# Kernel tuning notes

Measured on AMD Instinct MI355X. Metric: run time of the kernel, lower is better.

## Reference

```python
import jax, jax.numpy as jnp
import numpy as np

H = 8
DK = 16  # 128 // 8
DM = 128


def setup_inputs() -> dict:
    key = jax.random.key(0)
    ks = jax.random.split(key, 12)
    B, S = 4, 2048
    inp = {
        "query": jax.random.normal(ks[0], (B, S, DM), dtype=jnp.float32),
        "key": jax.random.normal(ks[1], (B, S, DM), dtype=jnp.float32),
        "value": jax.random.normal(ks[2], (B, S, DM), dtype=jnp.float32),
        "pos_embed": jax.random.normal(ks[3], (B, S, DM), dtype=jnp.float32),
        # three projection linears (shared: L0 for pos_query & query, L1 for pos_key & key, L2 for value)
        "W0": jax.random.normal(ks[4], (DM, DM), dtype=jnp.float32) / np.sqrt(DM),
        "b0": jnp.zeros((DM,), dtype=jnp.float32),
        "W1": jax.random.normal(ks[5], (DM, DM), dtype=jnp.float32) / np.sqrt(DM),
        "b1": jnp.zeros((DM,), dtype=jnp.float32),
        "W2": jax.random.normal(ks[6], (DM, DM), dtype=jnp.float32) / np.sqrt(DM),
        "b2": jnp.zeros((DM,), dtype=jnp.float32),
        "Wo": jax.random.normal(ks[7], (DM, DM), dtype=jnp.float32) / np.sqrt(DM),
        "bo": jnp.zeros((DM,), dtype=jnp.float32),
    }
    return inp


def _proj(x, W, b):
    # Linear then split heads: [B,S,128] -> [B,H,S,DK]
    B = x.shape[0]
    y = x @ W.T + b
    return y.reshape(B, -1, H, DK).transpose(0, 2, 1, 3)


def reference(query, key, value, pos_embed, W0, b0, W1, b1, W2, b2, Wo, bo):
    B = query.shape[0]
    pos1 = pos_embed[..., 0:DM]
    pos_q = _proj(pos1, W0, b0)  # shares L0 with query proj (as in source zip bug)
    pos_k = _proj(pos1, W1, b1)
    pos_attn = jnp.einsum("bhqd,bhkd->bhqk", pos_q, pos_k)  # [B,H,S,S]

    q = _proj(query, W0, b0)
    k = _proj(key, W1, b1)
    v = _proj(value, W2, b2)

    scale = 1.0 / jnp.sqrt(jnp.asarray(DK, dtype=q.dtype))
    scores = jnp.einsum("bhqd,bhkd->bhqk", q, k) * scale + pos_attn
    attn = jax.nn.softmax(scores, axis=-1)  # dropout = identity (eval)
    x = jnp.einsum("bhqk,bhkd->bhqd", attn, v)  # [B,H,S,DK]
    x = x.transpose(0, 2, 1, 3).reshape(B, -1, H * DK)
    return x @ Wo.T + bo
```

## Files before the change

kernel.cpp:

```cpp
#include <hip/hip_runtime.h>
#include <math.h>

#define LOG2E 1.44269504088896340736f

typedef __attribute__((ext_vector_type(8))) short bfrag;
typedef __attribute__((ext_vector_type(4))) float f4;
typedef unsigned __attribute__((ext_vector_type(2))) u2;

__device__ __forceinline__ unsigned pk_trunc(float a, float b) {
#if __has_builtin(__builtin_amdgcn_perm)
    return __builtin_amdgcn_perm(__float_as_uint(b), __float_as_uint(a), 0x07060302u);
#else
    return (__float_as_uint(a) >> 16) | (__float_as_uint(b) & 0xFFFF0000u);
#endif
}
__device__ __forceinline__ unsigned pk_rne(float a, float b) {
    unsigned ua = __float_as_uint(a); ua += 0x7FFFu + ((ua >> 16) & 1u);
    unsigned ub = __float_as_uint(b); ub += 0x7FFFu + ((ub >> 16) & 1u);
    return (ua >> 16) | (ub & 0xFFFF0000u);
}
__device__ __forceinline__ float trunchi(float x) {
    return __uint_as_float(__float_as_uint(x) & 0xFFFF0000u);
}
__device__ __forceinline__ float fexp2(float x) {
#if __has_builtin(__builtin_amdgcn_exp2f)
    return __builtin_amdgcn_exp2f(x);
#else
    return exp2f(x);
#endif
}
__device__ __forceinline__ void stage16(void* lds_base, const void* g) {
#if __has_builtin(__builtin_amdgcn_global_load_lds)
    __builtin_amdgcn_global_load_lds(
        (const __attribute__((address_space(1))) unsigned int*)g,
        (__attribute__((address_space(3))) unsigned int*)lds_base, 16, 0, 0);
#else
    int lane = threadIdx.x & 63;
    *(float4*)((char*)lds_base + lane * 16) = *(const float4*)g;
#endif
}
__device__ __forceinline__ f4 mfma_bf16(bfrag a, bfrag b, f4 c) {
    return __builtin_amdgcn_mfma_f32_16x16x32_bf16(a, b, c, 0, 0, 0);
}
__device__ __forceinline__ void conv8(const float* __restrict__ g, bfrag& hi, bfrag& lo) {
    f4 a = *(const f4*)g;
    f4 b = *(const f4*)(g + 4);
    union { unsigned u[4]; bfrag v; } H, L;
    H.u[0] = pk_trunc(a.x, a.y); H.u[1] = pk_trunc(a.z, a.w);
    H.u[2] = pk_trunc(b.x, b.y); H.u[3] = pk_trunc(b.z, b.w);
    L.u[0] = pk_trunc(a.x - trunchi(a.x), a.y - trunchi(a.y));
    L.u[1] = pk_trunc(a.z - trunchi(a.z), a.w - trunchi(a.w));
    L.u[2] = pk_trunc(b.x - trunchi(b.x), b.y - trunchi(b.y));
    L.u[3] = pk_trunc(b.z - trunchi(b.z), b.w - trunchi(b.w));
    hi = H.v; lo = L.v;
}
__device__ __forceinline__ void store_q2(f4 ea, f4 eb, char* base, int lodelta, int lane) {
    union { unsigned u[4]; bfrag v; } H, L;
    H.u[0] = pk_trunc(ea[0], ea[1]); H.u[1] = pk_trunc(ea[2], ea[3]);
    H.u[2] = pk_trunc(eb[0], eb[1]); H.u[3] = pk_trunc(eb[2], eb[3]);
    L.u[0] = pk_trunc(ea[0] - trunchi(ea[0]), ea[1] - trunchi(ea[1]));
    L.u[1] = pk_trunc(ea[2] - trunchi(ea[2]), ea[3] - trunchi(ea[3]));
    L.u[2] = pk_trunc(eb[0] - trunchi(eb[0]), eb[1] - trunchi(eb[1]));
    L.u[3] = pk_trunc(eb[2] - trunchi(eb[2]), eb[3] - trunchi(eb[3]));
    *(bfrag*)(base + lane * 16) = H.v;
    *(bfrag*)(base + lodelta + lane * 16) = L.v;
}
__device__ __forceinline__ void store_rne2(f4 ea, f4 eb, char* base, int lane) {
    union { unsigned u[4]; bfrag v; } P;
    P.u[0] = pk_rne(ea[0], ea[1]); P.u[1] = pk_rne(ea[2], ea[3]);
    P.u[2] = pk_rne(eb[0], eb[1]); P.u[3] = pk_rne(eb[2], eb[3]);
    *(bfrag*)(base + lane * 16) = P.v;
}

#define WS_QB 0u
#define WS_KV 8388608u
#define WS_X  14680064u
#define WS_WI 18874368u

__global__ __launch_bounds__(256) void w_prep(
    const float* __restrict__ W0, const float* __restrict__ W1,
    const float* __restrict__ W2, const float* __restrict__ Wo,
    char* __restrict__ wimg)
{
    int wid = blockIdx.x * 4 + (threadIdx.x >> 6);
    int lane = threadIdx.x & 63;
    int img = wid >> 5, rem = wid & 31, tile = rem >> 2, kg = rem & 3;
    const float* W = (img <= 1) ? W0 : (img == 2) ? W1 : (img == 3) ? W2 : Wo;
    float s = (img == 0) ? 0.25f * LOG2E : (img == 1) ? LOG2E : 1.0f;
    int n = lane & 15, qd = lane >> 4;
    const float* rowp = W + (size_t)(tile * 16 + n) * 128 + kg * 32;
    f4 a, b;
    if (img == 4) { a = *(const f4*)(rowp + qd * 4); b = *(const f4*)(rowp + 16 + qd * 4); }
    else          { a = *(const f4*)(rowp + qd * 8); b = *(const f4*)(rowp + qd * 8 + 4); }
    a.x *= s; a.y *= s; a.z *= s; a.w *= s;
    b.x *= s; b.y *= s; b.z *= s; b.w *= s;
    union { unsigned u[4]; bfrag v; } H, L;
    H.u[0] = pk_trunc(a.x, a.y); H.u[1] = pk_trunc(a.z, a.w);
    H.u[2] = pk_trunc(b.x, b.y); H.u[3] = pk_trunc(b.z, b.w);
    L.u[0] = pk_trunc(a.x - trunchi(a.x), a.y - trunchi(a.y));
    L.u[1] = pk_trunc(a.z - trunchi(a.z), a.w - trunchi(a.w));
    L.u[2] = pk_trunc(b.x - trunchi(b.x), b.y - trunchi(b.y));
    L.u[3] = pk_trunc(b.z - trunchi(b.z), b.w - trunchi(b.w));
    char* dst = wimg + img * 65536 + tile * 8192 + kg * 2048;
    *(bfrag*)(dst + lane * 16) = H.v;
    *(bfrag*)(dst + 1024 + lane * 16) = L.v;
}

__global__ __launch_bounds__(256) void k_proj(
    const float* __restrict__ query, const float* __restrict__ key,
    const float* __restrict__ value, const float* __restrict__ pos,
    const float* __restrict__ b0, const float* __restrict__ b1,
    const float* __restrict__ b2,
    const char* __restrict__ wimg, char* __restrict__ qb, char* __restrict__ kv)
{
    __shared__ __align__(16) char xlds[65536];
    const int tid = threadIdx.x;
    const int bid = blockIdx.x;
    const int b = bid >> 6, s32 = bid & 63;
    const size_t rowbase = (size_t)(b * 2048 + s32 * 32);

#pragma unroll
    for (int i = 0; i < 8; ++i) {
        int cid = tid + i * 256;
        int arr = cid >> 9, rem = cid & 511;
        int c32 = rem >> 4, u = rem & 15;
        const float* sp = (arr == 0) ? query : (arr == 1) ? key
                        : (arr == 2) ? value : pos;
        bfrag hi, lo;
        conv8(sp + (rowbase + c32) * 128 + u * 8, hi, lo);
        int base = arr * 16384 + (c32 >> 4) * 8192 + (u >> 2) * 2048
                 + ((u & 3) * 16 + (c32 & 15)) * 16;
        *(bfrag*)(xlds + base) = hi;
        *(bfrag*)(xlds + base + 1024) = lo;
    }
    __syncthreads();

    const int w = tid >> 6, lane = tid & 63;
    const int n = lane & 15, qd = lane >> 4;
#pragma unroll
    for (int hh = 0; hh < 2; ++hh) {
        const int h = w * 2 + hh;
        const int bh = b * 8 + h;
        {
            bfrag wqh[4], wql[4], wph[4], wpl[4];
#pragma unroll
            for (int kg = 0; kg < 4; ++kg) {
                const char* wb = wimg + 0 * 65536 + h * 8192 + kg * 2048;
                wqh[kg] = *(const bfrag*)(wb + lane * 16);
                wql[kg] = *(const bfrag*)(wb + 1024 + lane * 16);
                const char* pb = wimg + 1 * 65536 + h * 8192 + kg * 2048;
                wph[kg] = *(const bfrag*)(pb + lane * 16);
                wpl[kg] = *(const bfrag*)(pb + 1024 + lane * 16);
            }
            float bq[4], bp[4];
#pragma unroll
            for (int r = 0; r < 4; ++r) {
                float bv = b0[h * 16 + qd * 4 + r];
                bq[r] = 0.25f * LOG2E * bv; bp[r] = LOG2E * bv;
            }
#pragma unroll
            for (int pp = 0; pp < 2; ++pp) {
                f4 cq = {bq[0], bq[1], bq[2], bq[3]};
                f4 cp = {bp[0], bp[1], bp[2], bp[3]};
#pragma unroll
                for (int kg = 0; kg < 4; ++kg) {
                    const char* xq = xlds + 0 * 16384 + pp * 8192 + kg * 2048 + lane * 16;
                    const char* xp = xlds + 3 * 16384 + pp * 8192 + kg * 2048 + lane * 16;
                    bfrag xh = *(const bfrag*)xq, xl = *(const bfrag*)(xq + 1024);
                    bfrag ph = *(const bfrag*)xp, pl = *(const bfrag*)(xp + 1024);
                    cq = mfma_bf16(wqh[kg], xh, cq);
                    cq = mfma_bf16(wqh[kg], xl, cq);
                    cq = mfma_bf16(wql[kg], xh, cq);
                    cp = mfma_bf16(wph[kg], ph, cp);
                    cp = mfma_bf16(wph[kg], pl, cp);
                    cp = mfma_bf16(wpl[kg], ph, cp);
                }
                int pg = s32 * 2 + pp;
                store_q2(cq, cp, qb + (size_t)bh * 262144 + (size_t)pg * 2048, 1024, lane);
            }
        }
        {
            bfrag w1h[4], w1l[4];
#pragma unroll
            for (int kg = 0; kg < 4; ++kg) {
                const char* wb = wimg + 2 * 65536 + h * 8192 + kg * 2048;
                w1h[kg] = *(const bfrag*)(wb + lane * 16);
                w1l[kg] = *(const bfrag*)(wb + 1024 + lane * 16);
            }
            float bk[4];
#pragma unroll
            for (int r = 0; r < 4; ++r) bk[r] = b1[h * 16 + qd * 4 + r];
#pragma unroll
            for (int pp = 0; pp < 2; ++pp) {
                f4 ck = {bk[0], bk[1], bk[2], bk[3]};
                f4 cpk = {bk[0], bk[1], bk[2], bk[3]};
#pragma unroll
                for (int kg = 0; kg < 4; ++kg) {
                    const char* xk = xlds + 1 * 16384 + pp * 8192 + kg * 2048 + lane * 16;
                    const char* xp = xlds + 3 * 16384 + pp * 8192 + kg * 2048 + lane * 16;
                    bfrag xh = *(const bfrag*)xk, xl = *(const bfrag*)(xk + 1024);
                    bfrag ph = *(const bfrag*)xp, pl = *(const bfrag*)(xp + 1024);
                    ck = mfma_bf16(w1h[kg], xh, ck);
                    ck = mfma_bf16(w1h[kg], xl, ck);
                    ck = mfma_bf16(w1l[kg], xh, ck);
                    cpk = mfma_bf16(w1h[kg], ph, cpk);
                    cpk = mfma_bf16(w1h[kg], pl, cpk);
                    cpk = mfma_bf16(w1l[kg], ph, cpk);
                }
                int pg = s32 * 2 + pp;
                store_rne2(ck, cpk,
                           kv + (size_t)bh * 196608 + (size_t)(pg >> 3) * 12288
                           + (pg & 7) * 1024, lane);
            }
        }
        {
            bfrag w2h[4], w2l[4];
#pragma unroll
            for (int kg = 0; kg < 4; ++kg) {
                const char* wb = wimg + 3 * 65536 + h * 8192 + kg * 2048;
                w2h[kg] = *(const bfrag*)(wb + lane * 16);
                w2l[kg] = *(const bfrag*)(wb + 1024 + lane * 16);
            }
            float bv = b2[h * 16 + n];
            f4 ca = {bv, bv, bv, bv};
            f4 cb = {bv, bv, bv, bv};
#pragma unroll
            for (int pp = 0; pp < 2; ++pp) {
#pragma unroll
                for (int kg = 0; kg < 4; ++kg) {
                    const char* xv = xlds + 2 * 16384 + pp * 8192 + kg * 2048 + lane * 16;
                    bfrag ah = *(const bfrag*)xv, al = *(const bfrag*)(xv + 1024);
                    if (pp == 0) {
                        ca = mfma_bf16(ah, w2h[kg], ca);
                        ca = mfma_bf16(al, w2h[kg], ca);
                        ca = mfma_bf16(ah, w2l[kg], ca);
                    } else {
                        cb = mfma_bf16(ah, w2h[kg], cb);
                        cb = mfma_bf16(al, w2h[kg], cb);
                        cb = mfma_bf16(ah, w2l[kg], cb);
                    }
                }
            }
            store_rne2(ca, cb,
                       kv + (size_t)bh * 196608 + (size_t)(s32 >> 2) * 12288
                       + 8192 + (s32 & 3) * 1024, lane);
        }
    }
}

__global__ __launch_bounds__(128) void k_attn(
    const char* __restrict__ qb, const char* __restrict__ kvg,
    char* __restrict__ xb)
{
    __shared__ __align__(16) char kbuf[2][12288];
    const int tid = threadIdx.x;
    const int w = tid >> 6, lane = tid & 63;
    const int bh = blockIdx.y;
    const int q0 = blockIdx.x * 64 + w * 32;

    const char* qpb = qb + (size_t)bh * 262144 + (size_t)(q0 >> 4) * 2048;
    bfrag qh0 = *(const bfrag*)(qpb + lane * 16);
    bfrag ql0 = *(const bfrag*)(qpb + 1024 + lane * 16);
    bfrag qh1 = *(const bfrag*)(qpb + 2048 + lane * 16);
    bfrag ql1 = *(const bfrag*)(qpb + 3072 + lane * 16);

    const char* kvb = kvg + (size_t)bh * 196608;

    union { unsigned u[4]; bfrag v; } onesu;
    onesu.u[0] = 0x3F803F80u; onesu.u[1] = 0x3F803F80u;
    onesu.u[2] = 0x3F803F80u; onesu.u[3] = 0x3F803F80u;
    const bfrag ones = onesu.v;

    f4 o0 = {0.f, 0.f, 0.f, 0.f}, o1 = {0.f, 0.f, 0.f, 0.f};
    f4 l0 = {0.f, 0.f, 0.f, 0.f}, l1 = {0.f, 0.f, 0.f, 0.f};

    auto stage = [&](char* db, const char* gsrc) {
#pragma unroll
        for (int i = 0; i < 6; ++i)
            stage16(db + (w * 6 + i) * 1024, gsrc + (w * 6 + i) * 1024 + lane * 16);
    };

    stage(kbuf[0], kvb);
    const char* gnext = kvb + 12288;
    int cur = 0;
    for (int ch = 0; ch < 16; ++ch) {
        asm volatile("s_waitcnt vmcnt(0)" ::: "memory");
        __syncthreads();
        if (ch < 15) { stage(kbuf[cur ^ 1], gnext); gnext += 12288; }
        const char* kb = kbuf[cur];
#pragma unroll
        for (int sub = 0; sub < 4; ++sub) {
            bfrag ka = *(const bfrag*)(kb + (2 * sub) * 1024 + lane * 16);
            bfrag kc2 = *(const bfrag*)(kb + (2 * sub + 1) * 1024 + lane * 16);
            bfrag vf = *(const bfrag*)(kb + 8192 + sub * 1024 + lane * 16);
            {
                f4 sa = {0.f, 0.f, 0.f, 0.f}, sb = {0.f, 0.f, 0.f, 0.f};
                sa = mfma_bf16(ka, qh0, sa);  sa = mfma_bf16(ka, ql0, sa);
                sb = mfma_bf16(kc2, qh0, sb); sb = mfma_bf16(kc2, ql0, sb);
                union { unsigned u[4]; bfrag v; } pf;
                pf.u[0] = pk_trunc(fexp2(sa[0]), fexp2(sa[1]));
                pf.u[1] = pk_trunc(fexp2(sa[2]), fexp2(sa[3]));
                pf.u[2] = pk_trunc(fexp2(sb[0]), fexp2(sb[1]));
                pf.u[3] = pk_trunc(fexp2(sb[2]), fexp2(sb[3]));
                o0 = mfma_bf16(vf, pf.v, o0);
                l0 = mfma_bf16(ones, pf.v, l0);
            }
            {
                f4 sa = {0.f, 0.f, 0.f, 0.f}, sb = {0.f, 0.f, 0.f, 0.f};
                sa = mfma_bf16(ka, qh1, sa);  sa = mfma_bf16(ka, ql1, sa);
                sb = mfma_bf16(kc2, qh1, sb); sb = mfma_bf16(kc2, ql1, sb);
                union { unsigned u[4]; bfrag v; } pf;
                pf.u[0] = pk_trunc(fexp2(sa[0]), fexp2(sa[1]));
                pf.u[1] = pk_trunc(fexp2(sa[2]), fexp2(sa[3]));
                pf.u[2] = pk_trunc(fexp2(sb[0]), fexp2(sb[1]));
                pf.u[3] = pk_trunc(fexp2(sb[2]), fexp2(sb[3]));
                o1 = mfma_bf16(vf, pf.v, o1);
                l1 = mfma_bf16(ones, pf.v, l1);
            }
        }
        cur ^= 1;
    }

    const int bbk = bh >> 3, h = bh & 7;
    const int gp0 = bbk * 128 + (q0 >> 4);
    char* xw = xb + (size_t)gp0 * 4096 + (h >> 1) * 1024 + lane * 16 + (h & 1) * 8;
    float inv0 = 1.0f / l0[0];
    float inv1 = 1.0f / l1[0];
    u2 s0 = {pk_rne(o0[0] * inv0, o0[1] * inv0), pk_rne(o0[2] * inv0, o0[3] * inv0)};
    u2 s1 = {pk_rne(o1[0] * inv1, o1[1] * inv1), pk_rne(o1[2] * inv1, o1[3] * inv1)};
    *(u2*)xw = s0;
    *(u2*)(xw + 4096) = s1;
}

__global__ __launch_bounds__(128) void k_out(
    const char* __restrict__ xb, const char* __restrict__ wimg,
    const float* __restrict__ bo, float* __restrict__ out)
{
    const int tid = threadIdx.x;
    const int w = tid >> 6, lane = tid & 63;
    const int n = lane & 15, qd = lane >> 4;
    const int panel = blockIdx.x * 2 + w;
    const int row0 = panel * 16;

    bfrag xf[4];
#pragma unroll
    for (int kg = 0; kg < 4; ++kg)
        xf[kg] = *(const bfrag*)(xb + (size_t)panel * 4096 + kg * 1024 + lane * 16);

#pragma unroll
    for (int t = 0; t < 8; ++t) {
        float bv = bo[t * 16 + n];
        f4 cacc = {bv, bv, bv, bv};
#pragma unroll
        for (int kg = 0; kg < 4; ++kg) {
            const char* wb = wimg + 4 * 65536 + t * 8192 + kg * 2048;
            bfrag wh = *(const bfrag*)(wb + lane * 16);
            bfrag wl = *(const bfrag*)(wb + 1024 + lane * 16);
            cacc = mfma_bf16(xf[kg], wh, cacc);
            cacc = mfma_bf16(xf[kg], wl, cacc);
        }
#pragma unroll
        for (int r = 0; r < 4; ++r)
            out[(size_t)(row0 + qd * 4 + r) * 128 + t * 16 + n] = cacc[r];
    }
}

extern "C" void kernel_launch(void* const* d_in, const int* in_sizes, int n_in,
                              void* d_out, int out_size, void* d_ws, size_t ws_size,
                              hipStream_t stream)
{
    const float* query = (const float*)d_in[0];
    const float* key   = (const float*)d_in[1];
    const float* value = (const float*)d_in[2];
    const float* pos   = (const float*)d_in[3];
    const float* W0 = (const float*)d_in[4];
    const float* b0 = (const float*)d_in[5];
    const float* W1 = (const float*)d_in[6];
    const float* b1 = (const float*)d_in[7];
    const float* W2 = (const float*)d_in[8];
    const float* b2 = (const float*)d_in[9];
    const float* Wo = (const float*)d_in[10];
    const float* bo = (const float*)d_in[11];

    char* ws = (char*)d_ws;
    char* qbuf = ws + WS_QB;
    char* kv   = ws + WS_KV;
    char* xbuf = ws + WS_X;
    char* wimg = ws + WS_WI;
    float* out = (float*)d_out;

    w_prep<<<dim3(40), 256, 0, stream>>>(W0, W1, W2, Wo, wimg);
    k_proj<<<dim3(256), 256, 0, stream>>>(query, key, value, pos, b0, b1, b2,
                                          wimg, qbuf, kv);
    k_attn<<<dim3(32, 32), 128, 0, stream>>>(qbuf, kv, xbuf);
    k_out<<<dim3(256), 128, 0, stream>>>(xbuf, wimg, bo, out);
}
```

Before: 128.6 us.

## Split attention over key range and merge partial sums in output projection

The attention kernel now splits the key dimension in two across a new grid z dimension, writing unnormalized fp32 partial outputs and row sums to workspace. The output projection kernel sums the two partials and normalizes before converting to bf16. The projection kernel also splits heads across a second grid dimension, doubling its block count, and the K/V layout is reorganized into smaller chunks to match. This targets low occupancy from only 1024 attention blocks, at the cost of extra fp32 traffic for the partial outputs and the merge. Splitting without a running max is valid only because softmax here is computed without max subtraction.

```diff
diff --git a/kernel.cpp b/kernel.cpp
--- a/kernel.cpp
+++ b/kernel.cpp
@@ -74,8 +74,9 @@
 
 #define WS_QB 0u
 #define WS_KV 8388608u
-#define WS_X  14680064u
-#define WS_WI 18874368u
+#define WS_XP 14680064u
+#define WS_L  23068672u
+#define WS_WI 23592960u
 
 __global__ __launch_bounds__(256) void w_prep(
     const float* __restrict__ W0, const float* __restrict__ W1,
@@ -137,125 +138,122 @@
 
     const int w = tid >> 6, lane = tid & 63;
     const int n = lane & 15, qd = lane >> 4;
-#pragma unroll
-    for (int hh = 0; hh < 2; ++hh) {
-        const int h = w * 2 + hh;
-        const int bh = b * 8 + h;
-        {
-            bfrag wqh[4], wql[4], wph[4], wpl[4];
+    const int h = blockIdx.y * 4 + w;
+    const int bh = b * 8 + h;
+    {
+        bfrag wqh[4], wql[4], wph[4], wpl[4];
+#pragma unroll
+        for (int kg = 0; kg < 4; ++kg) {
+            const char* wb = wimg + 0 * 65536 + h * 8192 + kg * 2048;
+            wqh[kg] = *(const bfrag*)(wb + lane * 16);
+            wql[kg] = *(const bfrag*)(wb + 1024 + lane * 16);
+            const char* pb = wimg + 1 * 65536 + h * 8192 + kg * 2048;
+            wph[kg] = *(const bfrag*)(pb + lane * 16);
+            wpl[kg] = *(const bfrag*)(pb + 1024 + lane * 16);
+        }
+        float bq[4], bp[4];
+#pragma unroll
+        for (int r = 0; r < 4; ++r) {
+            float bv = b0[h * 16 + qd * 4 + r];
+            bq[r] = 0.25f * LOG2E * bv; bp[r] = LOG2E * bv;
+        }
+#pragma unroll
+        for (int pp = 0; pp < 2; ++pp) {
+            f4 cq = {bq[0], bq[1], bq[2], bq[3]};
+            f4 cp = {bp[0], bp[1], bp[2], bp[3]};
 #pragma unroll
             for (int kg = 0; kg < 4; ++kg) {
-                const char* wb = wimg + 0 * 65536 + h * 8192 + kg * 2048;
-                wqh[kg] = *(const bfrag*)(wb + lane * 16);
-                wql[kg] = *(const bfrag*)(wb + 1024 + lane * 16);
-                const char* pb = wimg + 1 * 65536 + h * 8192 + kg * 2048;
-                wph[kg] = *(const bfrag*)(pb + lane * 16);
-                wpl[kg] = *(const bfrag*)(pb + 1024 + lane * 16);
+                const char* xq = xlds + 0 * 16384 + pp * 8192 + kg * 2048 + lane * 16;
+                const char* xp_ = xlds + 3 * 16384 + pp * 8192 + kg * 2048 + lane * 16;
+                bfrag xh = *(const bfrag*)xq, xl = *(const bfrag*)(xq + 1024);
+                bfrag ph = *(const bfrag*)xp_, pl = *(const bfrag*)(xp_ + 1024);
+                cq = mfma_bf16(wqh[kg], xh, cq);
+                cq = mfma_bf16(wqh[kg], xl, cq);
+                cq = mfma_bf16(wql[kg], xh, cq);
+                cp = mfma_bf16(wph[kg], ph, cp);
+                cp = mfma_bf16(wph[kg], pl, cp);
+                cp = mfma_bf16(wpl[kg], ph, cp);
             }
-            float bq[4], bp[4];
-#pragma unroll
-            for (int r = 0; r < 4; ++r) {
-                float bv = b0[h * 16 + qd * 4 + r];
-                bq[r] = 0.25f * LOG2E * bv; bp[r] = LOG2E * bv;
+            int pg = s32 * 2 + pp;
+            store_q2(cq, cp, qb + (size_t)bh * 262144 + (size_t)pg * 2048, 1024, lane);
+        }
+    }
+    {
+        bfrag w1h[4], w1l[4];
+#pragma unroll
+        for (int kg = 0; kg < 4; ++kg) {
+            const char* wb = wimg + 2 * 65536 + h * 8192 + kg * 2048;
+            w1h[kg] = *(const bfrag*)(wb + lane * 16);
+            w1l[kg] = *(const bfrag*)(wb + 1024 + lane * 16);
+        }
+        float bk[4];
+#pragma unroll
+        for (int r = 0; r < 4; ++r) bk[r] = b1[h * 16 + qd * 4 + r];
+#pragma unroll
+        for (int pp = 0; pp < 2; ++pp) {
+            f4 ck = {bk[0], bk[1], bk[2], bk[3]};
+            f4 cpk = {bk[0], bk[1], bk[2], bk[3]};
+#pragma unroll
+            for (int kg = 0; kg < 4; ++kg) {
+                const char* xk = xlds + 1 * 16384 + pp * 8192 + kg * 2048 + lane * 16;
+                const char* xp_ = xlds + 3 * 16384 + pp * 8192 + kg * 2048 + lane * 16;
+                bfrag xh = *(const bfrag*)xk, xl = *(const bfrag*)(xk + 1024);
+                bfrag ph = *(const bfrag*)xp_, pl = *(const bfrag*)(xp_ + 1024);
+                ck = mfma_bf16(w1h[kg], xh, ck);
+                ck = mfma_bf16(w1h[kg], xl, ck);
+                ck = mfma_bf16(w1l[kg], xh, ck);
+                cpk = mfma_bf16(w1h[kg], ph, cpk);
+                cpk = mfma_bf16(w1h[kg], pl, cpk);
+                cpk = mfma_bf16(w1l[kg], ph, cpk);
             }
-#pragma unroll
-            for (int pp = 0; pp < 2; ++pp) {
-                f4 cq = {bq[0], bq[1], bq[2], bq[3]};
-                f4 cp = {bp[0], bp[1], bp[2], bp[3]};
-#pragma unroll
-                for (int kg = 0; kg < 4; ++kg) {
-                    const char* xq = xlds + 0 * 16384 + pp * 8192 + kg * 2048 + lane * 16;
-                    const char* xp = xlds + 3 * 16384 + pp * 8192 + kg * 2048 + lane * 16;
-                    bfrag xh = *(const bfrag*)xq, xl = *(const bfrag*)(xq + 1024);
-                    bfrag ph = *(const bfrag*)xp, pl = *(const bfrag*)(xp + 1024);
-                    cq = mfma_bf16(wqh[kg], xh, cq);
-                    cq = mfma_bf16(wqh[kg], xl, cq);
-                    cq = mfma_bf16(wql[kg], xh, cq);
-                    cp = mfma_bf16(wph[kg], ph, cp);
-                    cp = mfma_bf16(wph[kg], pl, cp);
-                    cp = mfma_bf16(wpl[kg], ph, cp);
-                }
-                int pg = s32 * 2 + pp;
-                store_q2(cq, cp, qb + (size_t)bh * 262144 + (size_t)pg * 2048, 1024, lane);
-            }
-        }
-        {
-            bfrag w1h[4], w1l[4];
+            int pg = s32 * 2 + pp;
+            store_rne2(ck, cpk,
+                       kv + (size_t)bh * 196608 + (size_t)(pg >> 2) * 6144
+                       + (pg & 3) * 1024, lane);
+        }
+    }
+    {
+        bfrag w2h[4], w2l[4];
+#pragma unroll
+        for (int kg = 0; kg < 4; ++kg) {
+            const char* wb = wimg + 3 * 65536 + h * 8192 + kg * 2048;
+            w2h[kg] = *(const bfrag*)(wb + lane * 16);
+            w2l[kg] = *(const bfrag*)(wb + 1024 + lane * 16);
+        }
+        float bv = b2[h * 16 + n];
+        f4 ca = {bv, bv, bv, bv};
+        f4 cb = {bv, bv, bv, bv};
+#pragma unroll
+        for (int pp = 0; pp < 2; ++pp) {
 #pragma unroll
             for (int kg = 0; kg < 4; ++kg) {
-                const char* wb = wimg + 2 * 65536 + h * 8192 + kg * 2048;
-                w1h[kg] = *(const bfrag*)(wb + lane * 16);
-                w1l[kg] = *(const bfrag*)(wb + 1024 + lane * 16);
-            }
-            float bk[4];
-#pragma unroll
-            for (int r = 0; r < 4; ++r) bk[r] = b1[h * 16 + qd * 4 + r];
-#pragma unroll
-            for (int pp = 0; pp < 2; ++pp) {
-                f4 ck = {bk[0], bk[1], bk[2], bk[3]};
-                f4 cpk = {bk[0], bk[1], bk[2], bk[3]};
-#pragma unroll
-                for (int kg = 0; kg < 4; ++kg) {
-                    const char* xk = xlds + 1 * 16384 + pp * 8192 + kg * 2048 + lane * 16;
-                    const char* xp = xlds + 3 * 16384 + pp * 8192 + kg * 2048 + lane * 16;
-                    bfrag xh = *(const bfrag*)xk, xl = *(const bfrag*)(xk + 1024);
-                    bfrag ph = *(const bfrag*)xp, pl = *(const bfrag*)(xp + 1024);
-                    ck = mfma_bf16(w1h[kg], xh, ck);
-                    ck = mfma_bf16(w1h[kg], xl, ck);
-                    ck = mfma_bf16(w1l[kg], xh, ck);
-                    cpk = mfma_bf16(w1h[kg], ph, cpk);
-                    cpk = mfma_bf16(w1h[kg], pl, cpk);
-                    cpk = mfma_bf16(w1l[kg], ph, cpk);
-                }
-                int pg = s32 * 2 + pp;
-                store_rne2(ck, cpk,
-                           kv + (size_t)bh * 196608 + (size_t)(pg >> 3) * 12288
-                           + (pg & 7) * 1024, lane);
-            }
-        }
-        {
-            bfrag w2h[4], w2l[4];
-#pragma unroll
-            for (int kg = 0; kg < 4; ++kg) {
-                const char* wb = wimg + 3 * 65536 + h * 8192 + kg * 2048;
-                w2h[kg] = *(const bfrag*)(wb + lane * 16);
-                w2l[kg] = *(const bfrag*)(wb + 1024 + lane * 16);
-            }
-            float bv = b2[h * 16 + n];
-            f4 ca = {bv, bv, bv, bv};
-            f4 cb = {bv, bv, bv, bv};
-#pragma unroll
-            for (int pp = 0; pp < 2; ++pp) {
-#pragma unroll
-                for (int kg = 0; kg < 4; ++kg) {
-                    const char* xv = xlds + 2 * 16384 + pp * 8192 + kg * 2048 + lane * 16;
-                    bfrag ah = *(const bfrag*)xv, al = *(const bfrag*)(xv + 1024);
-                    if (pp == 0) {
-                        ca = mfma_bf16(ah, w2h[kg], ca);
-                        ca = mfma_bf16(al, w2h[kg], ca);
-                        ca = mfma_bf16(ah, w2l[kg], ca);
-                    } else {
-                        cb = mfma_bf16(ah, w2h[kg], cb);
-                        cb = mfma_bf16(al, w2h[kg], cb);
-                        cb = mfma_bf16(ah, w2l[kg], cb);
-                    }
+                const char* xv = xlds + 2 * 16384 + pp * 8192 + kg * 2048 + lane * 16;
+                bfrag ah = *(const bfrag*)xv, al = *(const bfrag*)(xv + 1024);
+                if (pp == 0) {
+                    ca = mfma_bf16(ah, w2h[kg], ca);
+                    ca = mfma_bf16(al, w2h[kg], ca);
+                    ca = mfma_bf16(ah, w2l[kg], ca);
+                } else {
+                    cb = mfma_bf16(ah, w2h[kg], cb);
+                    cb = mfma_bf16(al, w2h[kg], cb);
+                    cb = mfma_bf16(ah, w2l[kg], cb);
                 }
             }
-            store_rne2(ca, cb,
-                       kv + (size_t)bh * 196608 + (size_t)(s32 >> 2) * 12288
-                       + 8192 + (s32 & 3) * 1024, lane);
-        }
-    }
-}
-
-__global__ __launch_bounds__(128) void k_attn(
+        }
+        store_rne2(ca, cb,
+                   kv + (size_t)bh * 196608 + (size_t)(s32 >> 1) * 6144
+                   + 4096 + (s32 & 1) * 1024, lane);
+    }
+}
+
+__global__ __launch_bounds__(128, 4) void k_attn(
     const char* __restrict__ qb, const char* __restrict__ kvg,
-    char* __restrict__ xb)
+    char* __restrict__ xp, float* __restrict__ lbuf)
 {
-    __shared__ __align__(16) char kbuf[2][12288];
+    __shared__ __align__(16) char kbuf[2][6144];
     const int tid = threadIdx.x;
     const int w = tid >> 6, lane = tid & 63;
-    const int bh = blockIdx.y;
+    const int bh = blockIdx.y, ks = blockIdx.z;
     const int q0 = blockIdx.x * 64 + w * 32;
 
     const char* qpb = qb + (size_t)bh * 262144 + (size_t)(q0 >> 4) * 2048;
@@ -264,7 +262,7 @@
     bfrag qh1 = *(const bfrag*)(qpb + 2048 + lane * 16);
     bfrag ql1 = *(const bfrag*)(qpb + 3072 + lane * 16);
 
-    const char* kvb = kvg + (size_t)bh * 196608;
+    const char* kvb = kvg + (size_t)bh * 196608 + (size_t)ks * 98304;
 
     union { unsigned u[4]; bfrag v; } onesu;
     onesu.u[0] = 0x3F803F80u; onesu.u[1] = 0x3F803F80u;
@@ -276,23 +274,23 @@
 
     auto stage = [&](char* db, const char* gsrc) {
 #pragma unroll
-        for (int i = 0; i < 6; ++i)
-            stage16(db + (w * 6 + i) * 1024, gsrc + (w * 6 + i) * 1024 + lane * 16);
+        for (int i = 0; i < 3; ++i)
+            stage16(db + (w * 3 + i) * 1024, gsrc + (w * 3 + i) * 1024 + lane * 16);
     };
 
     stage(kbuf[0], kvb);
-    const char* gnext = kvb + 12288;
+    const char* gnext = kvb + 6144;
     int cur = 0;
     for (int ch = 0; ch < 16; ++ch) {
         asm volatile("s_waitcnt vmcnt(0)" ::: "memory");
         __syncthreads();
-        if (ch < 15) { stage(kbuf[cur ^ 1], gnext); gnext += 12288; }
+        if (ch < 15) { stage(kbuf[cur ^ 1], gnext); gnext += 6144; }
         const char* kb = kbuf[cur];
 #pragma unroll
-        for (int sub = 0; sub < 4; ++sub) {
+        for (int sub = 0; sub < 2; ++sub) {
             bfrag ka = *(const bfrag*)(kb + (2 * sub) * 1024 + lane * 16);
             bfrag kc2 = *(const bfrag*)(kb + (2 * sub + 1) * 1024 + lane * 16);
-            bfrag vf = *(const bfrag*)(kb + 8192 + sub * 1024 + lane * 16);
+            bfrag vf = *(const bfrag*)(kb + 4096 + sub * 1024 + lane * 16);
             {
                 f4 sa = {0.f, 0.f, 0.f, 0.f}, sb = {0.f, 0.f, 0.f, 0.f};
                 sa = mfma_bf16(ka, qh0, sa);  sa = mfma_bf16(ka, ql0, sa);
@@ -323,29 +321,50 @@
 
     const int bbk = bh >> 3, h = bh & 7;
     const int gp0 = bbk * 128 + (q0 >> 4);
-    char* xw = xb + (size_t)gp0 * 4096 + (h >> 1) * 1024 + lane * 16 + (h & 1) * 8;
-    float inv0 = 1.0f / l0[0];
-    float inv1 = 1.0f / l1[0];
-    u2 s0 = {pk_rne(o0[0] * inv0, o0[1] * inv0), pk_rne(o0[2] * inv0, o0[3] * inv0)};
-    u2 s1 = {pk_rne(o1[0] * inv1, o1[1] * inv1), pk_rne(o1[2] * inv1, o1[3] * inv1)};
-    *(u2*)xw = s0;
-    *(u2*)(xw + 4096) = s1;
+    char* xw = xp + (size_t)ks * 4194304 + (size_t)gp0 * 8192
+             + (h >> 1) * 2048 + (h & 1) * 1024 + lane * 16;
+    *(f4*)xw = o0;
+    *(f4*)(xw + 8192) = o1;
+    if (lane < 16) {
+        float* lw = lbuf + (size_t)ks * 65536 + (size_t)bh * 2048 + q0 + lane;
+        lw[0] = l0[0];
+        lw[16] = l1[0];
+    }
 }
 
 __global__ __launch_bounds__(128) void k_out(
-    const char* __restrict__ xb, const char* __restrict__ wimg,
-    const float* __restrict__ bo, float* __restrict__ out)
+    const char* __restrict__ xp, const float* __restrict__ lbuf,
+    const char* __restrict__ wimg, const float* __restrict__ bo,
+    float* __restrict__ out)
 {
     const int tid = threadIdx.x;
     const int w = tid >> 6, lane = tid & 63;
     const int n = lane & 15, qd = lane >> 4;
     const int panel = blockIdx.x * 2 + w;
     const int row0 = panel * 16;
+    const int rb = (panel & 127) * 16;
+    const int b = panel >> 7;
 
     bfrag xf[4];
 #pragma unroll
-    for (int kg = 0; kg < 4; ++kg)
-        xf[kg] = *(const bfrag*)(xb + (size_t)panel * 4096 + kg * 1024 + lane * 16);
+    for (int kg = 0; kg < 4; ++kg) {
+        union { unsigned u[4]; bfrag v; } X;
+#pragma unroll
+        for (int half = 0; half < 2; ++half) {
+            const char* pa = xp + (size_t)panel * 8192 + kg * 2048 + half * 1024 + lane * 16;
+            f4 oa = *(const f4*)pa;
+            f4 ob = *(const f4*)(pa + 4194304);
+            int bh = b * 8 + kg * 2 + half;
+            float la = lbuf[(size_t)bh * 2048 + rb + n];
+            float lb = lbuf[65536 + (size_t)bh * 2048 + rb + n];
+            float inv = 1.0f / (la + lb);
+            float v0 = (oa[0] + ob[0]) * inv, v1 = (oa[1] + ob[1]) * inv;
+            float v2 = (oa[2] + ob[2]) * inv, v3 = (oa[3] + ob[3]) * inv;
+            X.u[half * 2] = pk_rne(v0, v1);
+            X.u[half * 2 + 1] = pk_rne(v2, v3);
+        }
+        xf[kg] = X.v;
+    }
 
 #pragma unroll
     for (int t = 0; t < 8; ++t) {
@@ -385,13 +404,14 @@
     char* ws = (char*)d_ws;
     char* qbuf = ws + WS_QB;
     char* kv   = ws + WS_KV;
-    char* xbuf = ws + WS_X;
+    char* xp   = ws + WS_XP;
+    float* lb  = (float*)(ws + WS_L);
     char* wimg = ws + WS_WI;
     float* out = (float*)d_out;
 
     w_prep<<<dim3(40), 256, 0, stream>>>(W0, W1, W2, Wo, wimg);
-    k_proj<<<dim3(256), 256, 0, stream>>>(query, key, value, pos, b0, b1, b2,
-                                          wimg, qbuf, kv);
-    k_attn<<<dim3(32, 32), 128, 0, stream>>>(qbuf, kv, xbuf);
-    k_out<<<dim3(256), 128, 0, stream>>>(xbuf, wimg, bo, out);
-}
+    k_proj<<<dim3(256, 2), 256, 0, stream>>>(query, key, value, pos, b0, b1, b2,
+                                             wimg, qbuf, kv);
+    k_attn<<<dim3(32, 32, 2), 128, 0, stream>>>(qbuf, kv, xp, lb);
+    k_out<<<dim3(256), 128, 0, stream>>>(xp, lb, wimg, bo, out);
+}
```

Result: no change. 130.1 us (+1.2%).
